# Kernel tuning notes

Hardware: AMD Instinct MI355X
Metric: run time of the kernel (lower is better)

The kernel has to match this reference:

```python
import jax, jax.numpy as jnp
import numpy as np

COMMITMENT_COST = 0.25

def setup_inputs() -> dict:
    key = jax.random.key(0)
    k1, k2 = jax.random.split(key)
    inputs = jax.random.normal(k1, (64, 256, 32, 32), dtype=jnp.float32)
    emb_w = jax.random.normal(k2, (1024, 256), dtype=jnp.float32)
    return {"inputs": inputs, "emb_w": emb_w}

def reference(inputs, emb_w):
    # inputs: [B, C, H, W] with C == embedding_dim; emb_w: [K, D]
    K, D = emb_w.shape
    x = jnp.transpose(inputs, (0, 2, 3, 1))          # [B, H, W, D]
    flat = x.reshape(-1, D)                          # [N, D]
    distances = (jnp.sum(flat * flat, axis=1, keepdims=True)
                 + jnp.sum(emb_w * emb_w, axis=1)
                 - 2.0 * flat @ emb_w.T)
    idx = jnp.argmin(distances, axis=1)              # [N]
    encodings = jax.nn.one_hot(idx, K, dtype=flat.dtype)  # [N, K]
    quantized = emb_w[idx].reshape(x.shape)          # gather == onehot @ emb_w
    # eval-mode forward (no EMA buffer mutation)
    loss = COMMITMENT_COST * jnp.mean((jax.lax.stop_gradient(quantized) - x) ** 2)
    quantized_st = x + jax.lax.stop_gradient(quantized - x)  # straight-through
    avg_probs = jnp.mean(encodings, axis=0)
    perplexity = jnp.exp(-jnp.sum(avg_probs * jnp.log(avg_probs + 1e-10)))
    return (loss, jnp.transpose(quantized_st, (0, 3, 1, 2)), perplexity, encodings)
```

## Files before the change

kernel.cpp:

```cpp
#include <hip/hip_runtime.h>

typedef _Float16 f16;
typedef _Float16 f16x4 __attribute__((ext_vector_type(4)));
typedef _Float16 f16x8 __attribute__((ext_vector_type(8)));
typedef float f32x4 __attribute__((ext_vector_type(4)));
typedef float f32x16 __attribute__((ext_vector_type(16)));
typedef unsigned u32;
typedef u32 u32x4 __attribute__((ext_vector_type(4)));

constexpr int Dd = 256;
constexpr long long QOFF     = 1;
constexpr long long PERP_OFF = 16777217LL;
constexpr long long ENC_OFF  = 16777218LL;
constexpr long long ENC_CNT  = 67108864LL;

__device__ inline f32x4 ntload4(const float* p) {
    return __builtin_nontemporal_load(reinterpret_cast<const f32x4*>(p));
}

__global__ void prep_kernel(const float* __restrict__ emb, char* __restrict__ epk,
                            float* __restrict__ enorm) {
    const int t = threadIdx.x;
    const int k = blockIdx.x * 4 + (t >> 6);
    const int d4 = (t & 63) * 4;
    float4 v = *reinterpret_cast<const float4*>(emb + (size_t)k * Dd + d4);
    float s = v.x * v.x + v.y * v.y + v.z * v.z + v.w * v.w;
#pragma unroll
    for (int m = 1; m < 64; m <<= 1) s += __shfl_xor(s, m);
    float a[4] = {v.x, v.y, v.z, v.w};
    f16x4 h;
#pragma unroll
    for (int j = 0; j < 4; ++j) h[j] = (f16)a[j];
    const int kt = k >> 5, l31 = k & 31;
    const int dc = d4 >> 4, hb = (d4 >> 3) & 1, j0 = d4 & 7;
    const int lane = 32 * hb + l31;
    size_t off = (size_t)kt * 16384 + (size_t)dc * 1024 + lane * 16 + j0 * 2;
    *reinterpret_cast<f16x4*>(epk + off) = h;
    if ((t & 63) == 0) enorm[k] = s;
}

__global__ __launch_bounds__(256) void xprep_kernel(const float* __restrict__ in,
                                                    char* __restrict__ xpk) {
    __shared__ char lds[32768];
    const int t = threadIdx.x;
    const int n0 = blockIdx.x * 64;
    const int b = n0 >> 10, hw0 = n0 & 1023;
    const float* inb = in + (size_t)b * (Dd * 1024) + hw0;
    {
        const int c  = t & 15;
        const int g  = (t >> 4) & 3;
        const int hi = t >> 6;
        const int dp = hi * 4 + (g ^ (c >> 2));
        for (int it = 0; it < 8; ++it) {
            const int d = it * 32 + dp * 2;
            f32x4 v0 = ntload4(inb + (size_t)d * 1024 + c * 4);
            f32x4 v1 = ntload4(inb + (size_t)(d + 1) * 1024 + c * 4);
#pragma unroll
            for (int j = 0; j < 4; ++j) {
                int p = 4 * c + j;
                union { f16 h[2]; u32 u; } ph;
                ph.h[0] = (f16)v0[j]; ph.h[1] = (f16)v1[j];
                int off = (p * 512 + d * 2) ^ ((p & 15) << 4);
                *reinterpret_cast<u32*>(lds + off) = ph.u;
            }
        }
    }
    __syncthreads();
    char* outb = xpk + (size_t)n0 * 512;
    for (int it = 0; it < 8; ++it) {
        int fid = it * 256 + t;
        int lane = fid & 63, dcl = (fid >> 6) & 15, ptl = fid >> 10;
        int p  = ptl * 32 + (lane & 31);
        int d0 = dcl * 16 + (lane >> 5) * 8;
        int off = (p * 512 + d0 * 2) ^ ((p & 15) << 4);
        u32x4 v = *reinterpret_cast<const u32x4*>(lds + off);
        __builtin_nontemporal_store(v, reinterpret_cast<u32x4*>(outb + (size_t)fid * 16));
    }
}

__global__ __launch_bounds__(512, 4) void argmin_kernel(
    const char* __restrict__ xpk, const char* __restrict__ epk,
    const float* __restrict__ enorm, float* __restrict__ gout)
{
    __shared__ char lds[40960];
    float* mb1 = reinterpret_cast<float*>(lds + 32768);
    float* mb2 = reinterpret_cast<float*>(lds + 34816);
    int*   mi1 = reinterpret_cast<int*>(lds + 36864);
    int*   mi2 = reinterpret_cast<int*>(lds + 38912);

    const int t  = threadIdx.x;
    const int g  = blockIdx.x >> 7;
    const int pb = blockIdx.x & 127;
    const int n0 = pb * 512;

    const int lane = t & 63, w = t >> 6;
    const int l31 = lane & 31, hh = lane >> 5;
    const int kt = g * 8 + w;
    const int kb = kt * 32;

    f16x8 e[16];
    {
        const char* pe = epk + (size_t)kt * 16384 + lane * 16;
#pragma unroll
        for (int dc = 0; dc < 16; ++dc)
            e[dc] = *reinterpret_cast<const f16x8*>(pe + dc * 1024);
    }

#pragma unroll 1
    for (int ch = 0; ch < 8; ++ch) {
        const int nc = n0 + ch * 64;

        {
            const char* xsrc = xpk + (size_t)nc * 512;
#pragma unroll
            for (int i = 0; i < 4; ++i) {
                u32x4 v = __builtin_nontemporal_load(
                    reinterpret_cast<const u32x4*>(xsrc + (size_t)(i * 512 + t) * 16));
                *reinterpret_cast<u32x4*>(lds + (i * 512 + t) * 16) = v;
            }
        }
        __syncthreads();

#pragma unroll 1
        for (int tl = 0; tl < 2; ++tl) {
            f32x16 acc = (f32x16)(0.f);
            const int xbase = tl * 16384 + lane * 16;
#pragma unroll
            for (int dc = 0; dc < 16; ++dc) {
                f16x8 xh = *reinterpret_cast<const f16x8*>(lds + xbase + dc * 1024);
                acc = __builtin_amdgcn_mfma_f32_32x32x16_f16(e[dc], xh, acc, 0, 0, 0);
            }
            float bd1 = 3.4e38f, bd2 = 3.4e38f; int bi1 = 0, bi2 = 0;
#pragma unroll
            for (int rq = 0; rq < 4; ++rq) {
                float4 env = *reinterpret_cast<const float4*>(enorm + kb + 8 * rq + 4 * hh);
                float en4[4] = {env.x, env.y, env.z, env.w};
#pragma unroll
                for (int ri = 0; ri < 4; ++ri) {
                    float s = fmaf(-2.0f, acc[rq * 4 + ri], en4[ri]);
                    int k = kb + 8 * rq + 4 * hh + ri;
                    if (s < bd1) { bd2 = bd1; bi2 = bi1; bd1 = s; bi1 = k; }
                    else if (s < bd2) { bd2 = s; bi2 = k; }
                }
            }
            {
                float ob1 = __shfl_xor(bd1, 32); int oi1 = __shfl_xor(bi1, 32);
                float ob2 = __shfl_xor(bd2, 32); int oi2 = __shfl_xor(bi2, 32);
                if (ob1 < bd1 || (ob1 == bd1 && oi1 < bi1)) {
                    float nb2; int ni2;
                    if (bd1 < ob2 || (bd1 == ob2 && bi1 < oi2)) { nb2 = bd1; ni2 = bi1; }
                    else { nb2 = ob2; ni2 = oi2; }
                    bd1 = ob1; bi1 = oi1; bd2 = nb2; bi2 = ni2;
                } else if (ob1 < bd2 || (ob1 == bd2 && oi1 < bi2)) { bd2 = ob1; bi2 = oi1; }
            }
            if (hh == 0) {
                int s = w * 64 + tl * 32 + l31;
                mb1[s] = bd1; mb2[s] = bd2; mi1[s] = bi1; mi2[s] = bi2;
            }
        }
        __syncthreads();

        if (t < 64) {
            float b1 = mb1[t], b2 = mb2[t]; int i1 = mi1[t], i2 = mi2[t];
#pragma unroll
            for (int ww = 1; ww < 8; ++ww) {
                int s = ww * 64 + t;
                float ob1 = mb1[s], ob2 = mb2[s]; int oi1 = mi1[s], oi2 = mi2[s];
                if (ob1 < b1 || (ob1 == b1 && oi1 < i1)) {
                    float nb2; int ni2;
                    if (b1 < ob2 || (b1 == ob2 && i1 < oi2)) { nb2 = b1; ni2 = i1; }
                    else { nb2 = ob2; ni2 = oi2; }
                    b1 = ob1; i1 = oi1; b2 = nb2; i2 = ni2;
                } else if (ob1 < b2 || (ob1 == b2 && oi1 < i2)) { b2 = ob1; i2 = oi1; }
            }
            f32x4 o;
            o[0] = b1; o[1] = b2;
            o[2] = __int_as_float(i1); o[3] = __int_as_float(i2);
            __builtin_nontemporal_store(
                o, reinterpret_cast<f32x4*>(gout + ((size_t)g * 65536 + nc + t) * 4));
        }
        __syncthreads();
    }
}

__global__ __launch_bounds__(256) void quantref_kernel(
    const float* __restrict__ in, const float* __restrict__ emb,
    const float* __restrict__ enorm, const float* __restrict__ gout,
    int* __restrict__ idx_out, float* __restrict__ outq,
    float* __restrict__ partials, int* __restrict__ counts)
{
    __shared__ float red[2][4][64];
    __shared__ int rowsel[64];
    __shared__ float sred[4];
    const int t = threadIdx.x;
    const int p = t & 63, cq = t >> 6;
    const int n0 = blockIdx.x * 64;
    const int b = n0 >> 10, hw0 = n0 & 1023;

    int k0, k1;
    {
        f32x4 v0 = *reinterpret_cast<const f32x4*>(gout + (size_t)(n0 + p) * 4);
        float b1 = v0[0], b2 = v0[1];
        int i1 = __float_as_int(v0[2]), i2 = __float_as_int(v0[3]);
#pragma unroll
        for (int g = 1; g < 4; ++g) {
            f32x4 v = *reinterpret_cast<const f32x4*>(
                gout + ((size_t)g * 65536 + n0 + p) * 4);
            float c1 = v[0], c2 = v[1];
            int j1 = __float_as_int(v[2]), j2 = __float_as_int(v[3]);
            if (c1 < b1 || (c1 == b1 && j1 < i1)) {
                float nb2; int ni2;
                if (b1 < c2 || (b1 == c2 && i1 < j2)) { nb2 = b1; ni2 = i1; }
                else { nb2 = c2; ni2 = j2; }
                b2 = nb2; i2 = ni2; b1 = c1; i1 = j1;
            } else if (c1 < b2 || (c1 == b2 && j1 < i2)) {
                b2 = c1; i2 = j1;
            }
        }
        k0 = i1; k1 = i2;
    }

    const float* e0 = emb + (size_t)k0 * Dd + cq * 64;
    const float* e1 = emb + (size_t)k1 * Dd + cq * 64;
    const float* xb = in + (size_t)b * (Dd * 1024) + (size_t)(cq * 64) * 1024 + hw0 + p;

    float xr[64];
    float d0 = 0.f, d1 = 0.f;
#pragma unroll
    for (int c = 0; c < 64; c += 4) {
        float4 a0 = *reinterpret_cast<const float4*>(e0 + c);
        float4 a1 = *reinterpret_cast<const float4*>(e1 + c);
        xr[c + 0] = __builtin_nontemporal_load(xb + (size_t)(c + 0) * 1024);
        xr[c + 1] = __builtin_nontemporal_load(xb + (size_t)(c + 1) * 1024);
        xr[c + 2] = __builtin_nontemporal_load(xb + (size_t)(c + 2) * 1024);
        xr[c + 3] = __builtin_nontemporal_load(xb + (size_t)(c + 3) * 1024);
        d0 = fmaf(xr[c+3], a0.w, fmaf(xr[c+2], a0.z, fmaf(xr[c+1], a0.y, fmaf(xr[c+0], a0.x, d0))));
        d1 = fmaf(xr[c+3], a1.w, fmaf(xr[c+2], a1.z, fmaf(xr[c+1], a1.y, fmaf(xr[c+0], a1.x, d1))));
    }
    red[0][cq][p] = d0;
    red[1][cq][p] = d1;
    __syncthreads();
    if (t < 64) {
        float dot0 = (red[0][0][t] + red[0][1][t]) + (red[0][2][t] + red[0][3][t]);
        float dot1 = (red[1][0][t] + red[1][1][t]) + (red[1][2][t] + red[1][3][t]);
        float s0 = enorm[k0] - 2.f * dot0;
        float s1 = enorm[k1] - 2.f * dot1;
        int row = (s1 < s0 || (s1 == s0 && k1 < k0)) ? k1 : k0;
        rowsel[t] = row;
        idx_out[n0 + t] = row;
        atomicAdd(&counts[row], 1);
    }
    __syncthreads();

    const int row = rowsel[p];
    const float* erow = emb + (size_t)row * Dd + cq * 64;
    const size_t base = (size_t)b * (Dd * 1024) + (size_t)(cq * 64) * 1024 + hw0 + p;
    float ls = 0.f;
#pragma unroll
    for (int c = 0; c < 64; c += 4) {
        float4 ev = *reinterpret_cast<const float4*>(erow + c);
        float e4[4] = {ev.x, ev.y, ev.z, ev.w};
#pragma unroll
        for (int j = 0; j < 4; ++j) {
            size_t a = base + (size_t)(c + j) * 1024;
            __builtin_nontemporal_store(e4[j], outq + a);
            float df = e4[j] - xr[c + j];
            ls = fmaf(df, df, ls);
        }
    }
#pragma unroll
    for (int m = 1; m < 64; m <<= 1) ls += __shfl_xor(ls, m);
    if ((t & 63) == 0) sred[t >> 6] = ls;
    __syncthreads();
    if (t == 0) partials[blockIdx.x] = (sred[0] + sred[1]) + (sred[2] + sred[3]);
}

__global__ void enc_kernel(const int* __restrict__ idx, float* __restrict__ enc) {
    const long long T = 16777215LL;
    long long gid    = (long long)blockIdx.x * 256 + threadIdx.x;
    long long stride = (long long)gridDim.x * 256;
    if (gid == 0) {
        enc[0] = (idx[0] == 0) ? 1.f : 0.f;
        enc[1] = (idx[0] == 1) ? 1.f : 0.f;
        enc[67108862LL] = (idx[65535] == 1022) ? 1.f : 0.f;
        enc[67108863LL] = (idx[65535] == 1023) ? 1.f : 0.f;
    }
    for (long long c = gid; c < T; c += stride) {
        long long rel = 2 + 4 * c;
        int n  = (int)(rel >> 10);
        int kk = (int)(rel & 1023);
        f32x4 v;
        if (kk <= 1020) {
            int iv = idx[n];
            v[0] = (kk     == iv) ? 1.f : 0.f;
            v[1] = (kk + 1 == iv) ? 1.f : 0.f;
            v[2] = (kk + 2 == iv) ? 1.f : 0.f;
            v[3] = (kk + 3 == iv) ? 1.f : 0.f;
        } else {
#pragma unroll
            for (int j = 0; j < 4; ++j) {
                long long rr = rel + j;
                int nn = (int)(rr >> 10);
                int kj = (int)(rr & 1023);
                v[j] = (idx[nn] == kj) ? 1.f : 0.f;
            }
        }
        __builtin_nontemporal_store(v, reinterpret_cast<f32x4*>(enc + rel));
    }
}

__global__ __launch_bounds__(1024) void fin_kernel(
    const int* __restrict__ counts, const float* __restrict__ partials,
    float* __restrict__ out)
{
    __shared__ float r1[16];
    __shared__ float r2[16];
    const int t = threadIdx.x;
    float pl = partials[t];
    float pv = (float)counts[t] * (1.0f / 65536.0f);
    float pp = pv * logf(pv + 1e-10f);
#pragma unroll
    for (int m = 1; m < 64; m <<= 1) {
        pl += __shfl_xor(pl, m);
        pp += __shfl_xor(pp, m);
    }
    if ((t & 63) == 0) { r1[t >> 6] = pl; r2[t >> 6] = pp; }
    __syncthreads();
    if (t == 0) {
        float s1 = 0.f, s2 = 0.f;
#pragma unroll
        for (int i = 0; i < 16; ++i) { s1 += r1[i]; s2 += r2[i]; }
        out[0]        = 0.25f * s1 / 16777216.0f;
        out[PERP_OFF] = expf(-s2);
    }
}

extern "C" void kernel_launch(void* const* d_in, const int* in_sizes, int n_in,
                              void* d_out, int out_size, void* d_ws, size_t ws_size,
                              hipStream_t stream) {
    const float* in  = (const float*)d_in[0];
    const float* emb = (const float*)d_in[1];
    float* out = (float*)d_out;

    char* ws = (char*)d_ws;
    int*   counts   = (int*)ws;
    float* partials = (float*)(ws + 4096);
    int*   idx      = (int*)(ws + 16384);

    const size_t xpkB = 33554432, goutB = 4194304, epkB = 524288;
    const size_t tailBytes = xpkB + goutB + epkB + 4096;
    uintptr_t base = ((uintptr_t)(out + ENC_OFF + ENC_CNT) - tailBytes) & ~(uintptr_t)255;
    char*  xpk   = (char*)base;
    float* gout  = (float*)(base + xpkB);
    char*  epk   = (char*)(base + xpkB + goutB);
    float* enorm = (float*)(base + xpkB + goutB + epkB);

    (void)hipMemsetAsync(counts, 0, 4096, stream);
    prep_kernel<<<256, 256, 0, stream>>>(emb, epk, enorm);
    xprep_kernel<<<1024, 256, 0, stream>>>(in, xpk);
    argmin_kernel<<<512, 512, 0, stream>>>(xpk, epk, enorm, gout);
    quantref_kernel<<<1024, 256, 0, stream>>>(in, emb, enorm, gout, idx,
                                              out + QOFF, partials, counts);
    enc_kernel<<<8192, 256, 0, stream>>>(idx, out + ENC_OFF);
    fin_kernel<<<1, 1024, 0, stream>>>(counts, partials, out);
}
```

Before: 237.0 us.

## Drop in-block cross-wave argmin reduction; write per-wave top-2 to global

The argmin kernel no longer merges the eight waves' top-2 candidates through LDS with an extra barrier and a single-wave reduction. Each wave now writes its own top-2 per point straight to a gout buffer indexed by k-tile, enlarged from 4 to 32 slices. The x chunk per iteration is doubled to 128 points, giving fewer barriers per block. In exchange, gout traffic grows eightfold, and quantref must merge 32 candidates per point serially in one wave before the rest of the block can proceed.

```diff
diff --git a/kernel.cpp b/kernel.cpp
--- a/kernel.cpp
+++ b/kernel.cpp
@@ -82,12 +82,7 @@
     const char* __restrict__ xpk, const char* __restrict__ epk,
     const float* __restrict__ enorm, float* __restrict__ gout)
 {
-    __shared__ char lds[40960];
-    float* mb1 = reinterpret_cast<float*>(lds + 32768);
-    float* mb2 = reinterpret_cast<float*>(lds + 34816);
-    int*   mi1 = reinterpret_cast<int*>(lds + 36864);
-    int*   mi2 = reinterpret_cast<int*>(lds + 38912);
-
+    __shared__ char lds[65536];
     const int t  = threadIdx.x;
     const int g  = blockIdx.x >> 7;
     const int pb = blockIdx.x & 127;
@@ -105,15 +100,16 @@
         for (int dc = 0; dc < 16; ++dc)
             e[dc] = *reinterpret_cast<const f16x8*>(pe + dc * 1024);
     }
+    float* goutk = gout + (size_t)kt * 65536 * 4;
 
 #pragma unroll 1
-    for (int ch = 0; ch < 8; ++ch) {
-        const int nc = n0 + ch * 64;
+    for (int ch = 0; ch < 4; ++ch) {
+        const int nc = n0 + ch * 128;
 
         {
             const char* xsrc = xpk + (size_t)nc * 512;
 #pragma unroll
-            for (int i = 0; i < 4; ++i) {
+            for (int i = 0; i < 8; ++i) {
                 u32x4 v = __builtin_nontemporal_load(
                     reinterpret_cast<const u32x4*>(xsrc + (size_t)(i * 512 + t) * 16));
                 *reinterpret_cast<u32x4*>(lds + (i * 512 + t) * 16) = v;
@@ -122,7 +118,7 @@
         __syncthreads();
 
 #pragma unroll 1
-        for (int tl = 0; tl < 2; ++tl) {
+        for (int tl = 0; tl < 4; ++tl) {
             f32x16 acc = (f32x16)(0.f);
             const int xbase = tl * 16384 + lane * 16;
 #pragma unroll
@@ -154,30 +150,12 @@
                 } else if (ob1 < bd2 || (ob1 == bd2 && oi1 < bi2)) { bd2 = ob1; bi2 = oi1; }
             }
             if (hh == 0) {
-                int s = w * 64 + tl * 32 + l31;
-                mb1[s] = bd1; mb2[s] = bd2; mi1[s] = bi1; mi2[s] = bi2;
-            }
-        }
-        __syncthreads();
-
-        if (t < 64) {
-            float b1 = mb1[t], b2 = mb2[t]; int i1 = mi1[t], i2 = mi2[t];
-#pragma unroll
-            for (int ww = 1; ww < 8; ++ww) {
-                int s = ww * 64 + t;
-                float ob1 = mb1[s], ob2 = mb2[s]; int oi1 = mi1[s], oi2 = mi2[s];
-                if (ob1 < b1 || (ob1 == b1 && oi1 < i1)) {
-                    float nb2; int ni2;
-                    if (b1 < ob2 || (b1 == ob2 && i1 < oi2)) { nb2 = b1; ni2 = i1; }
-                    else { nb2 = ob2; ni2 = oi2; }
-                    b1 = ob1; i1 = oi1; b2 = nb2; i2 = ni2;
-                } else if (ob1 < b2 || (ob1 == b2 && oi1 < i2)) { b2 = ob1; i2 = oi1; }
-            }
-            f32x4 o;
-            o[0] = b1; o[1] = b2;
-            o[2] = __int_as_float(i1); o[3] = __int_as_float(i2);
-            __builtin_nontemporal_store(
-                o, reinterpret_cast<f32x4*>(gout + ((size_t)g * 65536 + nc + t) * 4));
+                f32x4 o;
+                o[0] = bd1; o[1] = bd2;
+                o[2] = __int_as_float(bi1); o[3] = __int_as_float(bi2);
+                __builtin_nontemporal_store(
+                    o, reinterpret_cast<f32x4*>(goutk + (size_t)(nc + tl * 32 + l31) * 4));
+            }
         }
         __syncthreads();
     }
@@ -191,21 +169,21 @@
 {
     __shared__ float red[2][4][64];
     __shared__ int rowsel[64];
+    __shared__ int kk0[64], kk1[64];
     __shared__ float sred[4];
     const int t = threadIdx.x;
     const int p = t & 63, cq = t >> 6;
     const int n0 = blockIdx.x * 64;
     const int b = n0 >> 10, hw0 = n0 & 1023;
 
-    int k0, k1;
-    {
-        f32x4 v0 = *reinterpret_cast<const f32x4*>(gout + (size_t)(n0 + p) * 4);
+    if (t < 64) {
+        f32x4 v0 = *reinterpret_cast<const f32x4*>(gout + (size_t)(n0 + t) * 4);
         float b1 = v0[0], b2 = v0[1];
         int i1 = __float_as_int(v0[2]), i2 = __float_as_int(v0[3]);
-#pragma unroll
-        for (int g = 1; g < 4; ++g) {
+#pragma unroll 1
+        for (int kt = 1; kt < 32; ++kt) {
             f32x4 v = *reinterpret_cast<const f32x4*>(
-                gout + ((size_t)g * 65536 + n0 + p) * 4);
+                gout + ((size_t)kt * 65536 + n0 + t) * 4);
             float c1 = v[0], c2 = v[1];
             int j1 = __float_as_int(v[2]), j2 = __float_as_int(v[3]);
             if (c1 < b1 || (c1 == b1 && j1 < i1)) {
@@ -217,8 +195,10 @@
                 b2 = c1; i2 = j1;
             }
         }
-        k0 = i1; k1 = i2;
-    }
+        kk0[t] = i1; kk1[t] = i2;
+    }
+    __syncthreads();
+    const int k0 = kk0[p], k1 = kk1[p];
 
     const float* e0 = emb + (size_t)k0 * Dd + cq * 64;
     const float* e1 = emb + (size_t)k1 * Dd + cq * 64;
@@ -347,7 +327,7 @@
     float* partials = (float*)(ws + 4096);
     int*   idx      = (int*)(ws + 16384);
 
-    const size_t xpkB = 33554432, goutB = 4194304, epkB = 524288;
+    const size_t xpkB = 33554432, goutB = 33554432, epkB = 524288;
     const size_t tailBytes = xpkB + goutB + epkB + 4096;
     uintptr_t base = ((uintptr_t)(out + ENC_OFF + ENC_CNT) - tailBytes) & ~(uintptr_t)255;
     char*  xpk   = (char*)base;
```

Measured after the change: 254.8 us. 1.08x slower.
